# Kernel optimization log

Hardware: AMD Instinct MI355X
Metric: run time of the kernel (lower is better)

## Reference

```python
import jax, jax.numpy as jnp
import numpy as np

WINDOW_SIZE = 11
SIGMA = 1.5
C1 = 0.01 ** 2
C2 = 0.03 ** 2
L1_WEIGHT = 1.0
SSIM_WEIGHT = 1.0


def _gaussian_window(channels, window_size=WINDOW_SIZE, sigma=SIGMA):
    x = np.arange(window_size, dtype=np.float32) - window_size // 2
    g = np.exp(-(x ** 2) / (2.0 * sigma ** 2))
    g = g / g.sum()
    w2d = np.outer(g, g).astype(np.float32)  # [ws, ws]
    # depthwise kernel layout OIHW with I=1, O=channels
    return jnp.asarray(np.tile(w2d[None, None], (channels, 1, 1, 1)))


def _dwconv(x, w):
    pad = WINDOW_SIZE // 2
    return jax.lax.conv_general_dilated(
        x, w, window_strides=(1, 1), padding=[(pad, pad), (pad, pad)],
        dimension_numbers=('NCHW', 'OIHW', 'NCHW'),
        feature_group_count=x.shape[1])


def setup_inputs() -> dict:
    key = jax.random.key(0)
    k1, k2 = jax.random.split(key)
    shape = (16, 3, 512, 512)
    outputs = jax.random.uniform(k1, shape, dtype=jnp.float32)
    labels = jax.random.uniform(k2, shape, dtype=jnp.float32)
    return {"outputs": outputs, "labels": labels}


def reference(outputs, labels):
    img1, img2 = outputs, labels
    channel = img1.shape[1]
    window = _gaussian_window(channel).astype(img1.dtype)

    mu1 = _dwconv(img1, window)
    mu2 = _dwconv(img2, window)
    mu1_sq = mu1 * mu1
    mu2_sq = mu2 * mu2
    mu1_mu2 = mu1 * mu2
    sigma1_sq = _dwconv(img1 * img1, window) - mu1_sq
    sigma2_sq = _dwconv(img2 * img2, window) - mu2_sq
    sigma12 = _dwconv(img1 * img2, window) - mu1_mu2

    ssim_map = ((2 * mu1_mu2 + C1) * (2 * sigma12 + C2)) / (
        (mu1_sq + mu2_sq + C1) * (sigma1_sq + sigma2_sq + C2))
    ssim = jnp.mean(ssim_map)

    l1_loss = jnp.mean(jnp.abs(outputs - labels))
    ssim_loss = 1.0 - ssim
    return L1_WEIGHT * l1_loss + SSIM_WEIGHT * ssim_loss
```

## Files before the change

### kernel.cpp

```cpp
#include <hip/hip_runtime.h>
#include <hip/hip_bf16.h>
#include <math.h>

#define IMG 512
#define TW 64
#define TH 32
#define NTX 8
#define NTY 16
#define NIMG 48
#define NBLOCKS (NTX * NTY * NIMG)
#define NPIX (16LL * 3 * 512 * 512)

#define C1F 0.0001f
#define C2F 0.0009f


#define SR 84
#define SROWS 42
#define CHUNKF 256
#define NCHUNK 14
#define BUFFLOATS (NCHUNK * CHUNKF)

typedef __attribute__((ext_vector_type(4))) short short4v;
typedef __attribute__((ext_vector_type(8))) short short8;
typedef __attribute__((ext_vector_type(4))) float float4v;
typedef __attribute__((ext_vector_type(2))) unsigned uint2v;
typedef __attribute__((ext_vector_type(4))) unsigned uint4v;

__device__ __forceinline__ float4v mfma16(short4v a, short4v b, float4v c) {
#if defined(__HIP_DEVICE_COMPILE__)
    return __builtin_amdgcn_mfma_f32_16x16x16bf16_1k(a, b, c, 0, 0, 0);
#else
    return c;
#endif
}

__device__ __forceinline__ void gl_lds16(const float* g, float* l) {
#if defined(__HIP_DEVICE_COMPILE__)
    __builtin_amdgcn_global_load_lds(
        (const __attribute__((address_space(1))) void*)g,
        (__attribute__((address_space(3))) void*)l, 16, 0, 0);
#else
    (void)g; (void)l;
#endif
}

#define GW0 0.00102838f
#define GW1 0.00759877f
#define GW2 0.03600077f
#define GW3 0.10936069f
#define GW4 0.21300539f
#define GW5 0.26601172f

__device__ __forceinline__ unsigned short f2bf(float f) {
    unsigned u = __builtin_bit_cast(unsigned, f);
    u += 0x7FFF + ((u >> 16) & 1);
    return (unsigned short)(u >> 16);
}
__device__ __forceinline__ unsigned pk2(float a, float b) {
    __hip_bfloat162 h = __float22bfloat162_rn(make_float2(a, b));
    unsigned u;
    __builtin_memcpy(&u, &h, 4);
    return u;
}

#define BC4(U) __builtin_bit_cast(short4v, U)

#define HCONV_F32(ROWE, SROWE, DX, DY, DS, DP)                                 \
    {                                                                          \
        const int srow_ = (SROWE);                                             \
        const int b_ = (ROWE) * SR + co;                                       \
        float4v x0 = *(const float4v*)&xb[b_];                                 \
        float4v x1 = *(const float4v*)&xb[b_ + 4];                             \
        float4v y0 = *(const float4v*)&yb[b_];                                 \
        float4v y1 = *(const float4v*)&yb[b_ + 4];                             \
        uint4v ux_ = (uint4v){pk2(x0[0], x0[1]), pk2(x0[2], x0[3]),            \
                              pk2(x1[0], x1[1]), pk2(x1[2], x1[3])};           \
        uint4v uy_ = (uint4v){pk2(y0[0], y0[1]), pk2(y0[2], y0[3]),            \
                              pk2(y1[0], y1[1]), pk2(y1[2], y1[3])};           \
        uint4v u2_ = (uint4v){                                                 \
            pk2(fmaf(x0[0],x0[0],y0[0]*y0[0]), fmaf(x0[1],x0[1],y0[1]*y0[1])), \
            pk2(fmaf(x0[2],x0[2],y0[2]*y0[2]), fmaf(x0[3],x0[3],y0[3]*y0[3])), \
            pk2(fmaf(x1[0],x1[0],y1[0]*y1[0]), fmaf(x1[1],x1[1],y1[1]*y1[1])), \
            pk2(fmaf(x1[2],x1[2],y1[2]*y1[2]), fmaf(x1[3],x1[3],y1[3]*y1[3]))};\
        uint4v u3_ = (uint4v){                                                 \
            pk2(x0[0]*y0[0], x0[1]*y0[1]), pk2(x0[2]*y0[2], x0[3]*y0[3]),      \
            pk2(x1[0]*y1[0], x1[1]*y1[1]), pk2(x1[2]*y1[2], x1[3]*y1[3])};     \
        float4v d_;                                                            \
        d_ = __builtin_amdgcn_mfma_f32_16x16x32_bf16(                          \
                 __builtin_bit_cast(short8, ux_), bh, zero4, 0, 0, 0);         \
        DX = (uint2v){pk2(d_[0], d_[1]), pk2(d_[2], d_[3])};                   \
        d_ = __builtin_amdgcn_mfma_f32_16x16x32_bf16(                          \
                 __builtin_bit_cast(short8, uy_), bh, zero4, 0, 0, 0);         \
        DY = (uint2v){pk2(d_[0], d_[1]), pk2(d_[2], d_[3])};                   \
        d_ = __builtin_amdgcn_mfma_f32_16x16x32_bf16(                          \
                 __builtin_bit_cast(short8, u2_), bh, zero4, 0, 0, 0);         \
        DS = (uint2v){pk2(d_[0], d_[1]), pk2(d_[2], d_[3])};                   \
        d_ = __builtin_amdgcn_mfma_f32_16x16x32_bf16(                          \
                 __builtin_bit_cast(short8, u3_), bh, zero4, 0, 0, 0);         \
        DP = (uint2v){pk2(d_[0], d_[1]), pk2(d_[2], d_[3])};                   \
        if ((unsigned)(q - 1) <= 1u && (unsigned)(srow_ - 5) <= 31u)           \
            l1_loc += fabsf(x0[0]-y0[0])+fabsf(x0[1]-y0[1])                    \
                    + fabsf(x0[2]-y0[2])+fabsf(x0[3]-y0[3])                    \
                    + fabsf(x1[0]-y1[0])+fabsf(x1[1]-y1[1])                    \
                    + fabsf(x1[2]-y1[2])+fabsf(x1[3]-y1[3]);                   \
    }

#define SSIM_ACC(M1, M2, EE, PP)                                               \
    _Pragma("unroll")                                                          \
    for (int r_ = 0; r_ < 4; ++r_) {                                           \
        float mu1 = (M1)[r_], mu2 = (M2)[r_];                                  \
        float e   = (EE)[r_], e12 = (PP)[r_];                                  \
        float p = mu1 * mu2;                                                   \
        float s = fmaf(mu1, mu1, mu2 * mu2);                                   \
        float num1 = fmaf(2.f, p, C1F);                                        \
        float num2 = fmaf(2.f, e12 - p, C2F);                                  \
        float den1 = s + C1F;                                                  \
        float den2 = (e - s) + C2F;                                            \
        ssim_loc = fmaf(num1 * num2,                                           \
                        __builtin_amdgcn_rcpf(den1 * den2), ssim_loc);         \
    }

__global__ __launch_bounds__(256, 5)
void ssim_tile_kernel(const float* __restrict__ xg, const float* __restrict__ yg,
                      float* __restrict__ partials) {
    __shared__ float xb[BUFFLOATS];
    __shared__ float yb[BUFFLOATS];
    __shared__ unsigned short gwtbl[16];
    __shared__ float red[8];

    const int tid  = threadIdx.x;
    const int lane = tid & 63;
    const int w    = tid >> 6;
    const int q    = lane >> 4;
    const int n16  = lane & 15;

    const int img = blockIdx.z;
    const int r00  = blockIdx.y * TH - 5;
    const int c00a = blockIdx.x * TW - 8;
    const float* __restrict__ xi = xg + (size_t)img * (IMG * IMG);
    const float* __restrict__ yi = yg + (size_t)img * (IMG * IMG);

    if (tid < 16) {
        const float gwf[11] = {GW0, GW1, GW2, GW3, GW4, GW5, GW4, GW3, GW2, GW1, GW0};
        unsigned short v = 0;
        #pragma unroll
        for (int t = 0; t < 11; ++t)
            if (tid == t) v = f2bf(gwf[t]);
        gwtbl[tid] = v;
    }

    #pragma unroll
    for (int k = 0; k < 7; ++k) {
        const int ck = w * 7 + k;
        const bool isx = (ck < NCHUNK);
        const int c = isx ? ck : ck - NCHUNK;
        const int o = c * CHUNKF + lane * 4;
        const int row = o / SR;
        const int col = o - row * SR;
        const int gr = r00 + row, gc = c00a + col;
        if (((unsigned)gr < 512u) & ((unsigned)gc < 512u)) {
            const float* src = (isx ? xi : yi) + (size_t)gr * IMG + gc;
            float* dstb = (isx ? xb : yb) + c * CHUNKF;
            gl_lds16(src, dstb);
        }
    }

    const bool interior = ((unsigned)(blockIdx.x - 1) <= 5u) &
                          ((unsigned)(blockIdx.y - 1) <= 13u);
    if (!interior) {
        const float4v z4 = {0.f, 0.f, 0.f, 0.f};
        for (int o = tid * 4; o < BUFFLOATS; o += 1024) {
            int row = o / SR, col = o - row * SR;
            int gr = r00 + row, gc = c00a + col;
            if (!(((unsigned)gr < 512u) & ((unsigned)gc < 512u))) {
                *(float4v*)&xb[o] = z4;
                *(float4v*)&yb[o] = z4;
            }
        }
    }

    __syncthreads();

    short8 bh;
    short4v bv0, bv1;
    {
        int baseh = q * 8 - n16 - 3;
        #pragma unroll
        for (int j = 0; j < 8; ++j)
            bh[j] = (short)gwtbl[min((unsigned)(baseh + j), 15u)];
        int base0 = q * 4 - n16, base1 = q * 4 + 16 - n16;
        #pragma unroll
        for (int j = 0; j < 4; ++j) {
            bv0[j] = (short)gwtbl[min((unsigned)(base0 + j), 15u)];
            bv1[j] = (short)gwtbl[min((unsigned)(base1 + j), 15u)];
        }
    }

    const int co = w * 16 + q * 8;
    const float4v zero4 = {0.f, 0.f, 0.f, 0.f};
    float l1_loc = 0.f;
    uint2v d0x, d0y, d0s, d0p;
    uint2v e1x, e1y, e1s, e1p;
    uint2v f2x, f2y, f2s, f2p;
    HCONV_F32(n16,               n16,      d0x, d0y, d0s, d0p)
    HCONV_F32(16 + n16,          16 + n16, e1x, e1y, e1s, e1p)
    HCONV_F32(min(32 + n16, 41), 32 + n16, f2x, f2y, f2s, f2p)

    float ssim_loc = 0.f;
    {
        float4v am1 = mfma16(BC4(d0x), bv0, mfma16(BC4(e1x), bv1, zero4));
        float4v am2 = mfma16(BC4(d0y), bv0, mfma16(BC4(e1y), bv1, zero4));
        float4v ae  = mfma16(BC4(d0s), bv0, mfma16(BC4(e1s), bv1, zero4));
        float4v ap  = mfma16(BC4(d0p), bv0, mfma16(BC4(e1p), bv1, zero4));
        SSIM_ACC(am1, am2, ae, ap)
    }
    {
        float4v bm1 = mfma16(BC4(e1x), bv0, mfma16(BC4(f2x), bv1, zero4));
        float4v bm2 = mfma16(BC4(e1y), bv0, mfma16(BC4(f2y), bv1, zero4));
        float4v be  = mfma16(BC4(e1s), bv0, mfma16(BC4(f2s), bv1, zero4));
        float4v bp  = mfma16(BC4(e1p), bv0, mfma16(BC4(f2p), bv1, zero4));
        SSIM_ACC(bm1, bm2, be, bp)
    }

    #pragma unroll
    for (int off = 32; off > 0; off >>= 1) {
        ssim_loc += __shfl_down(ssim_loc, off);
        l1_loc   += __shfl_down(l1_loc, off);
    }
    if (lane == 0) {
        red[w] = ssim_loc;
        red[4 + w] = l1_loc;
    }
    __syncthreads();
    if (tid == 0) {
        float ss = red[0] + red[1] + red[2] + red[3];
        float ll = red[4] + red[5] + red[6] + red[7];
        int bid = blockIdx.x + NTX * (blockIdx.y + NTY * blockIdx.z);
        partials[bid] = ss;
        partials[NBLOCKS + bid] = ll;
    }
}

__global__ __launch_bounds__(1024)
void finalize_kernel(const float* __restrict__ partials, float* __restrict__ out) {
    __shared__ double rs[16], rl[16];
    const int tid = threadIdx.x;
    double ss = 0.0, ll = 0.0;
    for (int i = tid; i < NBLOCKS; i += 1024) {
        ss += (double)partials[i];
        ll += (double)partials[NBLOCKS + i];
    }
    #pragma unroll
    for (int off = 32; off > 0; off >>= 1) {
        ss += __shfl_down(ss, off);
        ll += __shfl_down(ll, off);
    }
    int wave = tid >> 6, lane = tid & 63;
    if (lane == 0) { rs[wave] = ss; rl[wave] = ll; }
    __syncthreads();
    if (tid == 0) {
        double sst = 0.0, llt = 0.0;
        #pragma unroll
        for (int w = 0; w < 16; ++w) { sst += rs[w]; llt += rl[w]; }
        double invn = 1.0 / (double)NPIX;
        out[0] = (float)(llt * invn + (1.0 - sst * invn));
    }
}

extern "C" void kernel_launch(void* const* d_in, const int* in_sizes, int n_in,
                              void* d_out, int out_size, void* d_ws, size_t ws_size,
                              hipStream_t stream) {
    const float* x = (const float*)d_in[0];
    const float* y = (const float*)d_in[1];
    float* out = (float*)d_out;
    float* partials = (float*)d_ws;

    dim3 grid(NTX, NTY, NIMG);
    ssim_tile_kernel<<<grid, dim3(256), 0, stream>>>(x, y, partials);
    finalize_kernel<<<1, dim3(1024), 0, stream>>>(partials, out);
}
```

Baseline: 129.5 us.

## Make SSIM kernel persistent with double-buffered LDS tile prefetch

Replaces the one-tile-per-block grid with 512 blocks that each walk 12 consecutive tiles. Shared-memory staging buffers are doubled so the next tile's global-to-LDS loads can be issued while the current tile's convolution and SSIM math run. The finalize kernel is shrunk to match the smaller partials array. The larger LDS footprint lowers blocks per CU from 5 to 2, which cuts the number of loads in flight and the latency hiding that comes from having many resident blocks.

```diff
diff --git a/kernel.cpp b/kernel.cpp
--- a/kernel.cpp
+++ b/kernel.cpp
@@ -8,7 +8,8 @@
 #define NTX 8
 #define NTY 16
 #define NIMG 48
-#define NBLOCKS (NTX * NTY * NIMG)
+#define TPB 12
+#define NPBLK 512
 #define NPIX (16LL * 3 * 512 * 512)
 
 #define C1F 0.0001f
@@ -66,14 +67,52 @@
 
 #define BC4(U) __builtin_bit_cast(short4v, U)
 
+#define TCOORD(TT, R00, C00A, XI, YI, BND)                                     \
+    {                                                                          \
+        const int gid_ = gbase + (TT);                                         \
+        XI = xg + ((size_t)(gid_ >> 7) * (IMG * IMG));                         \
+        YI = yg + ((size_t)(gid_ >> 7) * (IMG * IMG));                         \
+        const int by_ = (gid_ >> 3) & 15, bx_ = gid_ & 7;                      \
+        R00  = by_ * TH - 5;                                                   \
+        C00A = bx_ * TW - 8;                                                   \
+        BND  = !(((unsigned)(bx_ - 1) <= 5u) & ((unsigned)(by_ - 1) <= 13u));  \
+    }
+
+#define STAGE_ISSUE(B, R00, C00A, XI, YI)                                      \
+    _Pragma("unroll")                                                          \
+    for (int k_ = 0; k_ < 7; ++k_) {                                           \
+        const int ck_ = w * 7 + k_;                          \
+        const bool isx_ = (ck_ < NCHUNK);                                      \
+        const int c_ = isx_ ? ck_ : ck_ - NCHUNK;            \
+        const int o_ = c_ * CHUNKF + lane * 4;                                 \
+        const int row_ = o_ / SR;                                              \
+        const int col_ = o_ - row_ * SR;                                       \
+        const int gr_ = (R00) + row_, gc_ = (C00A) + col_;                     \
+        if (((unsigned)gr_ < 512u) & ((unsigned)gc_ < 512u)) {                 \
+            const float* src_ = (isx_ ? (XI) : (YI)) + (size_t)gr_ * IMG + gc_;\
+            float* dstb_ = (isx_ ? &xb[B][0] : &yb[B][0]) + c_ * CHUNKF;       \
+            gl_lds16(src_, dstb_);                                             \
+        }                                                                      \
+    }
+
+#define STAGE_ZERO(B, R00, C00A)                                               \
+    for (int o_ = tid * 4; o_ < BUFFLOATS; o_ += 1024) {                       \
+        const int row_ = o_ / SR, col_ = o_ - row_ * SR;                       \
+        const int gr_ = (R00) + row_, gc_ = (C00A) + col_;                     \
+        if (!(((unsigned)gr_ < 512u) & ((unsigned)gc_ < 512u))) {              \
+            *(float4v*)&xb[B][o_] = z4;                                        \
+            *(float4v*)&yb[B][o_] = z4;                                        \
+        }                                                                      \
+    }
+
 #define HCONV_F32(ROWE, SROWE, DX, DY, DS, DP)                                 \
     {                                                                          \
         const int srow_ = (SROWE);                                             \
         const int b_ = (ROWE) * SR + co;                                       \
-        float4v x0 = *(const float4v*)&xb[b_];                                 \
-        float4v x1 = *(const float4v*)&xb[b_ + 4];                             \
-        float4v y0 = *(const float4v*)&yb[b_];                                 \
-        float4v y1 = *(const float4v*)&yb[b_ + 4];                             \
+        float4v x0 = *(const float4v*)&xb[cur][b_];                            \
+        float4v x1 = *(const float4v*)&xb[cur][b_ + 4];                        \
+        float4v y0 = *(const float4v*)&yb[cur][b_];                            \
+        float4v y1 = *(const float4v*)&yb[cur][b_ + 4];                        \
         uint4v ux_ = (uint4v){pk2(x0[0], x0[1]), pk2(x0[2], x0[3]),            \
                               pk2(x1[0], x1[1]), pk2(x1[2], x1[3])};           \
         uint4v uy_ = (uint4v){pk2(y0[0], y0[1]), pk2(y0[2], y0[3]),            \
@@ -121,11 +160,11 @@
                         __builtin_amdgcn_rcpf(den1 * den2), ssim_loc);         \
     }
 
-__global__ __launch_bounds__(256, 5)
-void ssim_tile_kernel(const float* __restrict__ xg, const float* __restrict__ yg,
+__global__ __launch_bounds__(256, 2)
+void ssim_pipe_kernel(const float* __restrict__ xg, const float* __restrict__ yg,
                       float* __restrict__ partials) {
-    __shared__ float xb[BUFFLOATS];
-    __shared__ float yb[BUFFLOATS];
+    __shared__ float xb[2][BUFFLOATS];
+    __shared__ float yb[2][BUFFLOATS];
     __shared__ unsigned short gwtbl[16];
     __shared__ float red[8];
 
@@ -134,12 +173,6 @@
     const int w    = tid >> 6;
     const int q    = lane >> 4;
     const int n16  = lane & 15;
-
-    const int img = blockIdx.z;
-    const int r00  = blockIdx.y * TH - 5;
-    const int c00a = blockIdx.x * TW - 8;
-    const float* __restrict__ xi = xg + (size_t)img * (IMG * IMG);
-    const float* __restrict__ yi = yg + (size_t)img * (IMG * IMG);
 
     if (tid < 16) {
         const float gwf[11] = {GW0, GW1, GW2, GW3, GW4, GW5, GW4, GW3, GW2, GW1, GW0};
@@ -149,37 +182,6 @@
             if (tid == t) v = f2bf(gwf[t]);
         gwtbl[tid] = v;
     }
-
-    #pragma unroll
-    for (int k = 0; k < 7; ++k) {
-        const int ck = w * 7 + k;
-        const bool isx = (ck < NCHUNK);
-        const int c = isx ? ck : ck - NCHUNK;
-        const int o = c * CHUNKF + lane * 4;
-        const int row = o / SR;
-        const int col = o - row * SR;
-        const int gr = r00 + row, gc = c00a + col;
-        if (((unsigned)gr < 512u) & ((unsigned)gc < 512u)) {
-            const float* src = (isx ? xi : yi) + (size_t)gr * IMG + gc;
-            float* dstb = (isx ? xb : yb) + c * CHUNKF;
-            gl_lds16(src, dstb);
-        }
-    }
-
-    const bool interior = ((unsigned)(blockIdx.x - 1) <= 5u) &
-                          ((unsigned)(blockIdx.y - 1) <= 13u);
-    if (!interior) {
-        const float4v z4 = {0.f, 0.f, 0.f, 0.f};
-        for (int o = tid * 4; o < BUFFLOATS; o += 1024) {
-            int row = o / SR, col = o - row * SR;
-            int gr = r00 + row, gc = c00a + col;
-            if (!(((unsigned)gr < 512u) & ((unsigned)gc < 512u))) {
-                *(float4v*)&xb[o] = z4;
-                *(float4v*)&yb[o] = z4;
-            }
-        }
-    }
-
     __syncthreads();
 
     short8 bh;
@@ -197,30 +199,55 @@
         }
     }
 
+    const int gbase = blockIdx.x * TPB;
     const int co = w * 16 + q * 8;
     const float4v zero4 = {0.f, 0.f, 0.f, 0.f};
-    float l1_loc = 0.f;
-    uint2v d0x, d0y, d0s, d0p;
-    uint2v e1x, e1y, e1s, e1p;
-    uint2v f2x, f2y, f2s, f2p;
-    HCONV_F32(n16,               n16,      d0x, d0y, d0s, d0p)
-    HCONV_F32(16 + n16,          16 + n16, e1x, e1y, e1s, e1p)
-    HCONV_F32(min(32 + n16, 41), 32 + n16, f2x, f2y, f2s, f2p)
-
-    float ssim_loc = 0.f;
+    const float4v z4 = {0.f, 0.f, 0.f, 0.f};
+    float l1_loc = 0.f, ssim_loc = 0.f;
+
     {
-        float4v am1 = mfma16(BC4(d0x), bv0, mfma16(BC4(e1x), bv1, zero4));
-        float4v am2 = mfma16(BC4(d0y), bv0, mfma16(BC4(e1y), bv1, zero4));
-        float4v ae  = mfma16(BC4(d0s), bv0, mfma16(BC4(e1s), bv1, zero4));
-        float4v ap  = mfma16(BC4(d0p), bv0, mfma16(BC4(e1p), bv1, zero4));
-        SSIM_ACC(am1, am2, ae, ap)
-    }
-    {
-        float4v bm1 = mfma16(BC4(e1x), bv0, mfma16(BC4(f2x), bv1, zero4));
-        float4v bm2 = mfma16(BC4(e1y), bv0, mfma16(BC4(f2y), bv1, zero4));
-        float4v be  = mfma16(BC4(e1s), bv0, mfma16(BC4(f2s), bv1, zero4));
-        float4v bp  = mfma16(BC4(e1p), bv0, mfma16(BC4(f2p), bv1, zero4));
-        SSIM_ACC(bm1, bm2, be, bp)
+        const float *xi0, *yi0; int r00p, c00p; bool bnd0;
+        TCOORD(0, r00p, c00p, xi0, yi0, bnd0)
+        STAGE_ISSUE(0, r00p, c00p, xi0, yi0)
+        if (bnd0) STAGE_ZERO(0, r00p, c00p)
+    }
+    __syncthreads();
+
+    int cur = 0;
+    for (int t = 0; t < TPB; ++t) {
+        if (t + 1 < TPB) {
+            const float *nxi, *nyi; int nr00, nc00a; bool nbnd;
+            TCOORD(t + 1, nr00, nc00a, nxi, nyi, nbnd)
+            STAGE_ISSUE(cur ^ 1, nr00, nc00a, nxi, nyi)
+            if (nbnd) STAGE_ZERO(cur ^ 1, nr00, nc00a)
+        }
+
+        {
+            uint2v d0x, d0y, d0s, d0p;
+            uint2v e1x, e1y, e1s, e1p;
+            uint2v f2x, f2y, f2s, f2p;
+            HCONV_F32(n16,               n16,      d0x, d0y, d0s, d0p)
+            HCONV_F32(16 + n16,          16 + n16, e1x, e1y, e1s, e1p)
+            HCONV_F32(min(32 + n16, 41), 32 + n16, f2x, f2y, f2s, f2p)
+
+            {
+                float4v am1 = mfma16(BC4(d0x), bv0, mfma16(BC4(e1x), bv1, zero4));
+                float4v am2 = mfma16(BC4(d0y), bv0, mfma16(BC4(e1y), bv1, zero4));
+                float4v ae  = mfma16(BC4(d0s), bv0, mfma16(BC4(e1s), bv1, zero4));
+                float4v ap  = mfma16(BC4(d0p), bv0, mfma16(BC4(e1p), bv1, zero4));
+                SSIM_ACC(am1, am2, ae, ap)
+            }
+            {
+                float4v bm1 = mfma16(BC4(e1x), bv0, mfma16(BC4(f2x), bv1, zero4));
+                float4v bm2 = mfma16(BC4(e1y), bv0, mfma16(BC4(f2y), bv1, zero4));
+                float4v be  = mfma16(BC4(e1s), bv0, mfma16(BC4(f2s), bv1, zero4));
+                float4v bp  = mfma16(BC4(e1p), bv0, mfma16(BC4(f2p), bv1, zero4));
+                SSIM_ACC(bm1, bm2, be, bp)
+            }
+        }
+
+        __syncthreads();
+        cur ^= 1;
     }
 
     #pragma unroll
@@ -236,20 +263,19 @@
     if (tid == 0) {
         float ss = red[0] + red[1] + red[2] + red[3];
         float ll = red[4] + red[5] + red[6] + red[7];
-        int bid = blockIdx.x + NTX * (blockIdx.y + NTY * blockIdx.z);
-        partials[bid] = ss;
-        partials[NBLOCKS + bid] = ll;
-    }
-}
-
-__global__ __launch_bounds__(1024)
+        partials[blockIdx.x] = ss;
+        partials[NPBLK + blockIdx.x] = ll;
+    }
+}
+
+__global__ __launch_bounds__(256)
 void finalize_kernel(const float* __restrict__ partials, float* __restrict__ out) {
-    __shared__ double rs[16], rl[16];
+    __shared__ double rs[4], rl[4];
     const int tid = threadIdx.x;
     double ss = 0.0, ll = 0.0;
-    for (int i = tid; i < NBLOCKS; i += 1024) {
+    for (int i = tid; i < NPBLK; i += 256) {
         ss += (double)partials[i];
-        ll += (double)partials[NBLOCKS + i];
+        ll += (double)partials[NPBLK + i];
     }
     #pragma unroll
     for (int off = 32; off > 0; off >>= 1) {
@@ -260,9 +286,8 @@
     if (lane == 0) { rs[wave] = ss; rl[wave] = ll; }
     __syncthreads();
     if (tid == 0) {
-        double sst = 0.0, llt = 0.0;
-        #pragma unroll
-        for (int w = 0; w < 16; ++w) { sst += rs[w]; llt += rl[w]; }
+        double sst = rs[0] + rs[1] + rs[2] + rs[3];
+        double llt = rl[0] + rl[1] + rl[2] + rl[3];
         double invn = 1.0 / (double)NPIX;
         out[0] = (float)(llt * invn + (1.0 - sst * invn));
     }
@@ -276,7 +301,6 @@
     float* out = (float*)d_out;
     float* partials = (float*)d_ws;
 
-    dim3 grid(NTX, NTY, NIMG);
-    ssim_tile_kernel<<<grid, dim3(256), 0, stream>>>(x, y, partials);
-    finalize_kernel<<<1, dim3(1024), 0, stream>>>(partials, out);
-}
+    ssim_pipe_kernel<<<dim3(NPBLK), dim3(256), 0, stream>>>(x, y, partials);
+    finalize_kernel<<<1, dim3(256), 0, stream>>>(partials, out);
+}
```

Measured after the change: 131.7 us. No clear change (+1.7%).
